# Kernel tuning notes

Measured on AMD Instinct MI355X. Metric: run time of the kernel, lower is better.

The kernel has to match this reference:

```python
import jax, jax.numpy as jnp
import numpy as np

B, D, H, O = 32, 128, 256, 10


def setup_inputs() -> dict:
    key = jax.random.key(0)
    ks = jax.random.split(key, 8)
    return {
        "t": jax.random.uniform(ks[0], (1,), dtype=jnp.float32),
        "state_batch": jax.random.normal(ks[1], (2 * B, D), dtype=jnp.float32),
        "x0": jax.random.normal(ks[2], (B, D), dtype=jnp.float32),
        "x1": jax.random.normal(ks[3], (B, D), dtype=jnp.float32),
        "W1": jax.random.normal(ks[4], (D, H), dtype=jnp.float32) / np.sqrt(D),
        "b1": jax.random.normal(ks[5], (H,), dtype=jnp.float32) * 0.01,
        "W2": jax.random.normal(ks[6], (H, O), dtype=jnp.float32) / np.sqrt(H),
        "b2": jax.random.normal(ks[7], (O,), dtype=jnp.float32) * 0.01,
    }


def reference(t, state_batch, x0, x1, W1, b1, W2, b2):
    b = x0.shape[0]
    deviation, dev_velocity = state_batch[:b], state_batch[b:]  # [B,D] each
    tt = t[0]
    window = 4.0 * tt * (1.0 - tt)
    # point on the perturbed path
    x = x0 + tt * (x1 - x0) + window * deviation  # [B,D]

    def f_single(xs):  # [D] -> [O]
        return jnp.tanh(xs @ W1 + b1) @ W2 + b2

    def G_single(xs):  # [D] -> [D,D] pullback metric J^T J + eps I
        J = jax.jacrev(f_single)(xs)  # [O,D] (O small -> reverse mode)
        return J.T @ J + 1e-4 * jnp.eye(xs.shape[0], dtype=xs.dtype)

    # dG[b,i,j,k] = d G_ij / d x_k  -- replaces the torch double autograd loop
    dG = jax.vmap(jax.jacfwd(G_single))(x)  # [B,D,D,D]
    dG = dG / (jnp.sqrt(jnp.sum(dG * dG, axis=(1, 2, 3), keepdims=True)) + 1e-6)
    # Christoffel symbols (first kind, up to normalization as in source)
    Gamma = 0.5 * (dG + jnp.transpose(dG, (0, 2, 1, 3)) - jnp.transpose(dG, (0, 3, 1, 2)))
    a = -jnp.einsum('bijk,bj,bk->bi', Gamma, dev_velocity, dev_velocity)
    a = a / (jnp.linalg.norm(dev_velocity, axis=1, keepdims=True) + 1e-6)
    restoration = -0.1 * deviation
    return jnp.concatenate([dev_velocity, a + restoration], axis=0)  # [2B,D]
```

## Files before the change

### kernel.cpp

```cpp
#include <hip/hip_runtime.h>
#include <hip/hip_bf16.h>


#define NB 32

#define OP    0

__device__ int g_pdone = 0;
__device__ int g_bdone = 0;

template<int BF> __device__ __forceinline__ float ld(const void* p, int i) {
  if constexpr (BF) return __bfloat162float(((const __hip_bfloat16*)p)[i]);
  else return ((const float*)p)[i];
}
template<int BF> __device__ __forceinline__ void st(void* p, int i, float v) {
  if constexpr (BF) ((__hip_bfloat16*)p)[i] = __float2bfloat16(v);
  else ((float*)p)[i] = v;
}
__device__ __forceinline__ float b2f(unsigned short u) {
  return __uint_as_float(((unsigned int)u) << 16);
}
template<int BF> __device__ __forceinline__ void ld8v(const void* p, int i, float* o) {
  if constexpr (BF) {
    uint4 u = *(const uint4*)((const unsigned short*)p + i);
    o[0] = b2f((unsigned short)(u.x & 0xffff)); o[1] = b2f((unsigned short)(u.x >> 16));
    o[2] = b2f((unsigned short)(u.y & 0xffff)); o[3] = b2f((unsigned short)(u.y >> 16));
    o[4] = b2f((unsigned short)(u.z & 0xffff)); o[5] = b2f((unsigned short)(u.z >> 16));
    o[6] = b2f((unsigned short)(u.w & 0xffff)); o[7] = b2f((unsigned short)(u.w >> 16));
  } else {
    float4 a = *(const float4*)((const float*)p + i);
    float4 b = *(const float4*)((const float*)p + i + 4);
    o[0]=a.x; o[1]=a.y; o[2]=a.z; o[3]=a.w; o[4]=b.x; o[5]=b.y; o[6]=b.z; o[7]=b.w;
  }
}

__device__ __forceinline__ int blocksniff(const void* sb, int* sh) {
  if (threadIdx.x == 0) *sh = 0;
  __syncthreads();
  float v = fabsf(__bfloat162float(((const __hip_bfloat16*)sb)[threadIdx.x & 255]));
  if (!(v < 1000.0f)) atomicOr(sh, 1);
  __syncthreads();
  return (*sh == 0) ? 1 : 0;
}

#define LXS   0
#define LVS   128
#define LW2   256
#define LYS   2816
#define LRED  2832
#define LF1   2880
#define LEL   4416
#define LSW2  7488
#define LCL   10560
#define LCL2  10660
#define LW2P  10760
#define LTOT  13832

#define F1ACC(wv, gidx) do { \
    const float* sp_ = &sm[LSW2 + (gidx)*12]; \
    float4 s0_ = *(const float4*)sp_; \
    float4 s1_ = *(const float4*)(sp_+4); \
    float2 s2_ = *(const float2*)(sp_+8); \
    fa[0]+=(wv)*s0_.x; fa[1]+=(wv)*s0_.y; fa[2]+=(wv)*s0_.z; fa[3]+=(wv)*s0_.w; \
    fa[4]+=(wv)*s1_.x; fa[5]+=(wv)*s1_.y; fa[6]+=(wv)*s1_.z; fa[7]+=(wv)*s1_.w; \
    fa[8]+=(wv)*s2_.x; fa[9]+=(wv)*s2_.y; \
  } while (0)

template<int BF>
__device__ void fk_body(const void* tin, const void* sbin, const void* x0in,
                        const void* x1in, const void* W1in, const void* b1in,
                        const void* W2in, void* out, float* ws, float* sm) {
  int bid = blockIdx.x, t = threadIdx.x;
  if (bid >= NB) {
    int row = bid - NB;
    float* colh = sm;
    if (t < 128) colh[t] = ld<BF>(W1in, t * 256 + row);
    __syncthreads();
    float pacc = 0.f;
    for (int d = 0; d < 128; d += 4) {
      float4 c4 = *(const float4*)&colh[d];
      pacc += c4.x * ld<BF>(W1in, (d + 0) * 256 + t);
      pacc += c4.y * ld<BF>(W1in, (d + 1) * 256 + t);
      pacc += c4.z * ld<BF>(W1in, (d + 2) * 256 + t);
      pacc += c4.w * ld<BF>(W1in, (d + 3) * 256 + t);
    }
    __hip_atomic_store(&ws[OP + row * 256 + t], pacc,
                       __ATOMIC_RELAXED, __HIP_MEMORY_SCOPE_AGENT);
    __syncthreads();
    if (t == 0)
      __hip_atomic_fetch_add(&g_pdone, 1, __ATOMIC_RELAXED, __HIP_MEMORY_SCOPE_AGENT);
    return;
  }
  int b = bid;
  int w = t >> 6;
  float tt = ld<BF>(tin, 0);
  float window = 4.f * tt * (1.f - tt);
  if (t < 128) {
    float dev = ld<BF>(sbin, b * 128 + t);
    float v   = ld<BF>(sbin, (NB + b) * 128 + t);
    float x0v = ld<BF>(x0in, b * 128 + t);
    float x1v = ld<BF>(x1in, b * 128 + t);
    sm[LXS + t] = x0v + tt * (x1v - x0v) + window * dev;
    sm[LVS + t] = v;
  }
  for (int i = t; i < 2560; i += 256) sm[LW2 + i] = ld<BF>(W2in, i);
  __syncthreads();
  float hacc = ld<BF>(b1in, t), wacc = 0.f;
  for (int d = 0; d < 128; d += 4) {
    float4 xv = *(const float4*)&sm[LXS + d];
    float4 vv = *(const float4*)&sm[LVS + d];
    float w0 = ld<BF>(W1in, (d + 0) * 256 + t);
    float w1 = ld<BF>(W1in, (d + 1) * 256 + t);
    float w2 = ld<BF>(W1in, (d + 2) * 256 + t);
    float w3 = ld<BF>(W1in, (d + 3) * 256 + t);
    hacc += w0 * xv.x + w1 * xv.y + w2 * xv.z + w3 * xv.w;
    wacc += w0 * vv.x + w1 * vv.y + w2 * vv.z + w3 * vv.w;
  }
  float z  = tanhf(hacc);
  float sg = 1.f - z * z;
  float ug = -2.f * z * sg;
  float w2r[10];
  #pragma unroll
  for (int o = 0; o < 10; ++o) w2r[o] = sm[LW2 + t * 10 + o];
  #pragma unroll
  for (int o = 0; o < 10; ++o) sm[LSW2 + t * 12 + o] = sg * w2r[o];
  for (int i = t; i < 3072; i += 256) {
    int r = i / 12, c = i - r * 12;
    sm[LW2P + i] = (c < 10) ? sm[LW2 + r * 10 + c] : 0.f;
  }
  float cval = ug * wacc * wacc;
  float rv[11];
  #pragma unroll
  for (int o = 0; o < 10; ++o) rv[o] = cval * w2r[o];
  rv[10] = (t < 128) ? sm[LVS + t] * sm[LVS + t] : 0.f;
  #pragma unroll
  for (int o = 0; o < 11; ++o) {
    float v = rv[o];
    #pragma unroll
    for (int m = 32; m > 0; m >>= 1) v += __shfl_xor(v, m);
    if ((t & 63) == 0) sm[LRED + w * 12 + o] = v;
  }
  __syncthreads();
  if (t < 11) {
    float s = sm[LRED + t] + sm[LRED + 12 + t] + sm[LRED + 24 + t] + sm[LRED + 36 + t];
    if (t < 10) sm[LYS + t] = s;
    else        sm[LYS + 10] = sqrtf(s);
  }
  int half = t >> 7, r = t & 127;
  float fa[10];
  #pragma unroll
  for (int o = 0; o < 10; ++o) fa[o] = 0.f;
  {
    const int gbase = half * 128;
    for (int gg = 0; gg < 128; gg += 8) {
      int g = gbase + gg;
      float wv[8];
      ld8v<BF>(W1in, r * 256 + g, wv);
      F1ACC(wv[0], g + 0); F1ACC(wv[1], g + 1);
      F1ACC(wv[2], g + 2); F1ACC(wv[3], g + 3);
      F1ACC(wv[4], g + 4); F1ACC(wv[5], g + 5);
      F1ACC(wv[6], g + 6); F1ACC(wv[7], g + 7);
    }
  }
  if (half) {
    #pragma unroll
    for (int o = 0; o < 10; ++o) sm[LF1 + r * 12 + o] = fa[o];
  }
  __syncthreads();
  float aun = 0.f;
  if (!half) {
    #pragma unroll
    for (int o = 0; o < 10; ++o) {
      float f = fa[o] + sm[LF1 + r * 12 + o];
      sm[LF1 + r * 12 + o] = f;
      aun += f * sm[LYS + o];
    }
  }
  __syncthreads();
  float er[10];
  #pragma unroll
  for (int o = 0; o < 10; ++o) er[o] = 0.f;
  for (int d = 0; d < 128; ++d) {
    float w1v = ld<BF>(W1in, d * 256 + t);
    const float* fp = &sm[LF1 + d * 12];
    float4 a0 = *(const float4*)fp;
    float4 a1 = *(const float4*)(fp + 4);
    float2 a2 = *(const float2*)(fp + 8);
    er[0] += w1v * a0.x; er[1] += w1v * a0.y; er[2] += w1v * a0.z; er[3] += w1v * a0.w;
    er[4] += w1v * a1.x; er[5] += w1v * a1.y; er[6] += w1v * a1.z; er[7] += w1v * a1.w;
    er[8] += w1v * a2.x; er[9] += w1v * a2.y;
  }
  #pragma unroll
  for (int o = 0; o < 10; ++o) sm[LEL + t * 12 + o] = er[o];
  sm[LEL + t * 12 + 10] = ug;
  sm[LEL + t * 12 + 11] = 0.f;
  __syncthreads();
  float cpart = 0.f;
  if (t < 200) {
    int gh = (t >= 100) ? 1 : 0;
    int idx = t - gh * 100;
    int o = idx / 10, p = idx - o * 10;
    const float* sa = &sm[LSW2 + gh * 1536 + o];
    const float* sb = &sm[LEL  + gh * 1536 + p];
    #pragma unroll 4
    for (int g = 0; g < 128; ++g) cpart += sa[g * 12] * sb[g * 12];
    if (gh) sm[LCL2 + idx] = cpart;
  }
  __syncthreads();
  if (t < 100) sm[LCL + t] = cpart + sm[LCL2 + t];
  __syncthreads();
  float cwr[10];
  #pragma unroll
  for (int o = 0; o < 10; ++o) {
    float cw = 0.f;
    #pragma unroll
    for (int p = 0; p < 10; ++p) cw += sm[LCL + o * 10 + p] * w2r[p];
    cwr[o] = cw;
  }
  if (t == 0) {
    while (__hip_atomic_load(&g_pdone, __ATOMIC_RELAXED, __HIP_MEMORY_SCOPE_AGENT) < 256)
      __builtin_amdgcn_s_sleep(2);
  }
  __syncthreads();
  float acc = 0.f;
  for (int i0 = 0; i0 < 64; i0 += 16) {
    float ph[16];
    #pragma unroll
    for (int j = 0; j < 16; ++j)
      ph[j] = ws[OP + (w * 64 + i0 + j) * 256 + t];
    #pragma unroll
    for (int j = 0; j < 16; ++j) {
      int h = w * 64 + i0 + j;
      const float* rp = &sm[LEL + h * 12];
      float4 E0 = *(const float4*)rp;
      float4 E1 = *(const float4*)(rp + 4);
      float4 E2 = *(const float4*)(rp + 8);
      const float* wp = &sm[LW2P + h * 12];
      float4 W0 = *(const float4*)wp;
      float4 W1v = *(const float4*)(wp + 4);
      float4 W2v = *(const float4*)(wp + 8);
      float R = E0.x*w2r[0] + E0.y*w2r[1] + E0.z*w2r[2] + E0.w*w2r[3]
              + E1.x*w2r[4] + E1.y*w2r[5] + E1.z*w2r[6] + E1.w*w2r[7]
              + E2.x*w2r[8] + E2.y*w2r[9];
      float Rt = W0.x*er[0] + W0.y*er[1] + W0.z*er[2] + W0.w*er[3]
               + W1v.x*er[4] + W1v.y*er[5] + W1v.z*er[6] + W1v.w*er[7]
               + W2v.x*er[8] + W2v.y*er[9];
      float Qd = W0.x*cwr[0] + W0.y*cwr[1] + W0.z*cwr[2] + W0.w*cwr[3]
               + W1v.x*cwr[4] + W1v.y*cwr[5] + W1v.z*cwr[6] + W1v.w*cwr[7]
               + W2v.x*cwr[8] + W2v.y*cwr[9];
      acc += E2.z * ph[j] * (ph[j] * Qd + R * Rt);
    }
  }
  acc *= ug;
  #pragma unroll
  for (int m = 32; m > 0; m >>= 1) acc += __shfl_xor(acc, m);
  if ((t & 63) == 0) sm[LRED + w] = acc;
  __syncthreads();
  float F = sqrtf(fmaxf(2.f * (sm[LRED] + sm[LRED+1] + sm[LRED+2] + sm[LRED+3]), 0.f));
  float denom = (F + 1e-6f) * (sm[LYS + 10] + 1e-6f);
  if (t < 128) {
    st<BF>(out, b * 128 + t, ld<BF>(sbin, (NB + b) * 128 + t));
    float dev = ld<BF>(sbin, b * 128 + t);
    float val = -aun / denom - 0.1f * dev;
    st<BF>(out, (NB + b) * 128 + t, val);
  }
  __syncthreads();
  if (t == 0) {
    int old = __hip_atomic_fetch_add(&g_bdone, 1, __ATOMIC_RELAXED, __HIP_MEMORY_SCOPE_AGENT);
    if (old == NB - 1) {
      __hip_atomic_store(&g_pdone, 0, __ATOMIC_RELAXED, __HIP_MEMORY_SCOPE_AGENT);
      __hip_atomic_store(&g_bdone, 0, __ATOMIC_RELAXED, __HIP_MEMORY_SCOPE_AGENT);
    }
  }
}

__global__ __launch_bounds__(256, 2) void FK(const void* tin, const void* sbin,
                                             const void* x0in, const void* x1in,
                                             const void* W1in, const void* b1in,
                                             const void* W2in, void* out, float* ws) {
  __shared__ int sh;
  __shared__ __align__(16) float sm[LTOT];
  int bf = blocksniff(sbin, &sh);
  if (bf) fk_body<1>(tin, sbin, x0in, x1in, W1in, b1in, W2in, out, ws, sm);
  else    fk_body<0>(tin, sbin, x0in, x1in, W1in, b1in, W2in, out, ws, sm);
}

extern "C" void kernel_launch(void* const* d_in, const int* in_sizes, int n_in,
                              void* d_out, int out_size, void* d_ws, size_t ws_size,
                              hipStream_t stream) {
  float* ws = (float*)d_ws;
  const void* tin  = d_in[0];
  const void* sbin = d_in[1];
  const void* x0in = d_in[2];
  const void* x1in = d_in[3];
  const void* W1in = d_in[4];
  const void* b1in = d_in[5];
  const void* W2in = d_in[6];

  FK<<<dim3(NB + 256), dim3(256), 0, stream>>>(tin, sbin, x0in, x1in, W1in, b1in, W2in, d_out, ws);
}
```

Before: 99.54 us.

## Double block size to 512 threads and split reductions across thread halves

Blocks grow from 256 to 512 threads. Every per-batch phase (first-layer matvec, F1 accumulation, the er backprop loop, the Cl contraction, the final Hessian-weighted sum) now splits its reduction dimension across the extra thread groups, with partial sums combined through shared memory. Helper blocks that precompute W1^T W1 each handle two rows, so there are half as many of them and the spin-wait threshold changes to match. The aim is shorter serial loops per thread in the 32 latency-bound batch blocks, at the cost of more barriers, more shared-memory traffic and a tighter register budget.

```diff
diff --git a/kernel.cpp b/kernel.cpp
--- a/kernel.cpp
+++ b/kernel.cpp
@@ -3,8 +3,7 @@
 
 
 #define NB 32
-
-#define OP    0
+#define OP 0
 
 __device__ int g_pdone = 0;
 __device__ int g_bdone = 0;
@@ -48,13 +47,14 @@
 #define LW2   256
 #define LYS   2816
 #define LRED  2832
-#define LF1   2880
-#define LEL   4416
-#define LSW2  7488
-#define LCL   10560
-#define LCL2  10660
-#define LW2P  10760
-#define LTOT  13832
+#define LHW   2928
+#define LF1   3440
+#define LEL   4976
+#define LSW2  8048
+#define LCL   11120
+#define LCQ   11220
+#define LW2P  11520
+#define LTOT  14592
 
 #define F1ACC(wv, gidx) do { \
     const float* sp_ = &sm[LSW2 + (gidx)*12]; \
@@ -72,19 +72,24 @@
                         const void* W2in, void* out, float* ws, float* sm) {
   int bid = blockIdx.x, t = threadIdx.x;
   if (bid >= NB) {
-    int row = bid - NB;
+    int row0 = (bid - NB) * 2;
     float* colh = sm;
-    if (t < 128) colh[t] = ld<BF>(W1in, t * 256 + row);
+    if (t < 256) {
+      int qq = t >> 7, d = t & 127;
+      colh[qq * 128 + d] = ld<BF>(W1in, d * 256 + row0 + qq);
+    }
     __syncthreads();
+    int q = t >> 8, c = t & 255;
+    const float* ch = &colh[q * 128];
     float pacc = 0.f;
     for (int d = 0; d < 128; d += 4) {
-      float4 c4 = *(const float4*)&colh[d];
-      pacc += c4.x * ld<BF>(W1in, (d + 0) * 256 + t);
-      pacc += c4.y * ld<BF>(W1in, (d + 1) * 256 + t);
-      pacc += c4.z * ld<BF>(W1in, (d + 2) * 256 + t);
-      pacc += c4.w * ld<BF>(W1in, (d + 3) * 256 + t);
-    }
-    __hip_atomic_store(&ws[OP + row * 256 + t], pacc,
+      float4 c4 = *(const float4*)&ch[d];
+      pacc += c4.x * ld<BF>(W1in, (d + 0) * 256 + c);
+      pacc += c4.y * ld<BF>(W1in, (d + 1) * 256 + c);
+      pacc += c4.z * ld<BF>(W1in, (d + 2) * 256 + c);
+      pacc += c4.w * ld<BF>(W1in, (d + 3) * 256 + c);
+    }
+    __hip_atomic_store(&ws[OP + (row0 + q) * 256 + c], pacc,
                        __ATOMIC_RELAXED, __HIP_MEMORY_SCOPE_AGENT);
     __syncthreads();
     if (t == 0)
@@ -92,7 +97,11 @@
     return;
   }
   int b = bid;
-  int w = t >> 6;
+  int t2 = t & 255;
+  int q  = t >> 8;
+  int w  = t >> 6;
+  int r  = t & 127;
+  int qr = t >> 7;
   float tt = ld<BF>(tin, 0);
   float window = 4.f * tt * (1.f - tt);
   if (t < 128) {
@@ -103,42 +112,48 @@
     sm[LXS + t] = x0v + tt * (x1v - x0v) + window * dev;
     sm[LVS + t] = v;
   }
-  for (int i = t; i < 2560; i += 256) sm[LW2 + i] = ld<BF>(W2in, i);
-  __syncthreads();
-  float hacc = ld<BF>(b1in, t), wacc = 0.f;
-  for (int d = 0; d < 128; d += 4) {
-    float4 xv = *(const float4*)&sm[LXS + d];
-    float4 vv = *(const float4*)&sm[LVS + d];
-    float w0 = ld<BF>(W1in, (d + 0) * 256 + t);
-    float w1 = ld<BF>(W1in, (d + 1) * 256 + t);
-    float w2 = ld<BF>(W1in, (d + 2) * 256 + t);
-    float w3 = ld<BF>(W1in, (d + 3) * 256 + t);
-    hacc += w0 * xv.x + w1 * xv.y + w2 * xv.z + w3 * xv.w;
-    wacc += w0 * vv.x + w1 * vv.y + w2 * vv.z + w3 * vv.w;
-  }
-  float z  = tanhf(hacc);
-  float sg = 1.f - z * z;
-  float ug = -2.f * z * sg;
+  for (int i = t; i < 2560; i += 512) sm[LW2 + i] = ld<BF>(W2in, i);
+  __syncthreads();
+  float hp = q ? 0.f : ld<BF>(b1in, t2), wp = 0.f;
+  {
+    int d0 = q * 64;
+    for (int d = d0; d < d0 + 64; d += 4) {
+      float4 xv = *(const float4*)&sm[LXS + d];
+      float4 vv = *(const float4*)&sm[LVS + d];
+      float w0 = ld<BF>(W1in, (d + 0) * 256 + t2);
+      float w1 = ld<BF>(W1in, (d + 1) * 256 + t2);
+      float w2 = ld<BF>(W1in, (d + 2) * 256 + t2);
+      float w3 = ld<BF>(W1in, (d + 3) * 256 + t2);
+      hp += w0 * xv.x + w1 * xv.y + w2 * xv.z + w3 * xv.w;
+      wp += w0 * vv.x + w1 * vv.y + w2 * vv.z + w3 * vv.w;
+    }
+  }
+  if (q) { sm[LHW + t2 * 2] = hp; sm[LHW + t2 * 2 + 1] = wp; }
   float w2r[10];
   #pragma unroll
-  for (int o = 0; o < 10; ++o) w2r[o] = sm[LW2 + t * 10 + o];
-  #pragma unroll
-  for (int o = 0; o < 10; ++o) sm[LSW2 + t * 12 + o] = sg * w2r[o];
-  for (int i = t; i < 3072; i += 256) {
-    int r = i / 12, c = i - r * 12;
-    sm[LW2P + i] = (c < 10) ? sm[LW2 + r * 10 + c] : 0.f;
-  }
-  float cval = ug * wacc * wacc;
-  float rv[11];
-  #pragma unroll
-  for (int o = 0; o < 10; ++o) rv[o] = cval * w2r[o];
-  rv[10] = (t < 128) ? sm[LVS + t] * sm[LVS + t] : 0.f;
-  #pragma unroll
-  for (int o = 0; o < 11; ++o) {
-    float v = rv[o];
-    #pragma unroll
-    for (int m = 32; m > 0; m >>= 1) v += __shfl_xor(v, m);
-    if ((t & 63) == 0) sm[LRED + w * 12 + o] = v;
+  for (int o = 0; o < 10; ++o) w2r[o] = sm[LW2 + t2 * 10 + o];
+  __syncthreads();
+  float ug = 0.f;
+  if (!q) {
+    float hacc = hp + sm[LHW + t2 * 2];
+    float wacc = wp + sm[LHW + t2 * 2 + 1];
+    float z  = tanhf(hacc);
+    float sg = 1.f - z * z;
+    ug = -2.f * z * sg;
+    #pragma unroll
+    for (int o = 0; o < 10; ++o) sm[LSW2 + t2 * 12 + o] = sg * w2r[o];
+    float cval = ug * wacc * wacc;
+    float rv[11];
+    #pragma unroll
+    for (int o = 0; o < 10; ++o) rv[o] = cval * w2r[o];
+    rv[10] = (t < 128) ? sm[LVS + t] * sm[LVS + t] : 0.f;
+    #pragma unroll
+    for (int o = 0; o < 11; ++o) {
+      float v = rv[o];
+      #pragma unroll
+      for (int m = 32; m > 0; m >>= 1) v += __shfl_xor(v, m);
+      if ((t & 63) == 0) sm[LRED + w * 12 + o] = v;
+    }
   }
   __syncthreads();
   if (t < 11) {
@@ -146,13 +161,12 @@
     if (t < 10) sm[LYS + t] = s;
     else        sm[LYS + 10] = sqrtf(s);
   }
-  int half = t >> 7, r = t & 127;
   float fa[10];
   #pragma unroll
   for (int o = 0; o < 10; ++o) fa[o] = 0.f;
   {
-    const int gbase = half * 128;
-    for (int gg = 0; gg < 128; gg += 8) {
+    int gbase = qr * 64;
+    for (int gg = 0; gg < 64; gg += 8) {
       int g = gbase + gg;
       float wv[8];
       ld8v<BF>(W1in, r * 256 + g, wv);
@@ -162,16 +176,23 @@
       F1ACC(wv[6], g + 6); F1ACC(wv[7], g + 7);
     }
   }
-  if (half) {
-    #pragma unroll
-    for (int o = 0; o < 10; ++o) sm[LF1 + r * 12 + o] = fa[o];
+  if (qr == 1) {
+    #pragma unroll
+    for (int o = 0; o < 10; ++o) sm[LEL + r * 12 + o] = fa[o];
+  } else if (qr == 2) {
+    #pragma unroll
+    for (int o = 0; o < 10; ++o) sm[LEL + 1536 + r * 12 + o] = fa[o];
+  } else if (qr == 3) {
+    #pragma unroll
+    for (int o = 0; o < 10; ++o) sm[LW2P + r * 12 + o] = fa[o];
   }
   __syncthreads();
   float aun = 0.f;
-  if (!half) {
+  if (!qr) {
     #pragma unroll
     for (int o = 0; o < 10; ++o) {
-      float f = fa[o] + sm[LF1 + r * 12 + o];
+      float f = fa[o] + sm[LEL + r * 12 + o] + sm[LEL + 1536 + r * 12 + o]
+                      + sm[LW2P + r * 12 + o];
       sm[LF1 + r * 12 + o] = f;
       aun += f * sm[LYS + o];
     }
@@ -180,34 +201,50 @@
   float er[10];
   #pragma unroll
   for (int o = 0; o < 10; ++o) er[o] = 0.f;
-  for (int d = 0; d < 128; ++d) {
-    float w1v = ld<BF>(W1in, d * 256 + t);
-    const float* fp = &sm[LF1 + d * 12];
-    float4 a0 = *(const float4*)fp;
-    float4 a1 = *(const float4*)(fp + 4);
-    float2 a2 = *(const float2*)(fp + 8);
-    er[0] += w1v * a0.x; er[1] += w1v * a0.y; er[2] += w1v * a0.z; er[3] += w1v * a0.w;
-    er[4] += w1v * a1.x; er[5] += w1v * a1.y; er[6] += w1v * a1.z; er[7] += w1v * a1.w;
-    er[8] += w1v * a2.x; er[9] += w1v * a2.y;
-  }
-  #pragma unroll
-  for (int o = 0; o < 10; ++o) sm[LEL + t * 12 + o] = er[o];
-  sm[LEL + t * 12 + 10] = ug;
-  sm[LEL + t * 12 + 11] = 0.f;
-  __syncthreads();
+  {
+    int d0 = q * 64;
+    for (int d = d0; d < d0 + 64; ++d) {
+      float w1v = ld<BF>(W1in, d * 256 + t2);
+      const float* fp = &sm[LF1 + d * 12];
+      float4 a0 = *(const float4*)fp;
+      float4 a1 = *(const float4*)(fp + 4);
+      float2 a2 = *(const float2*)(fp + 8);
+      er[0] += w1v * a0.x; er[1] += w1v * a0.y; er[2] += w1v * a0.z; er[3] += w1v * a0.w;
+      er[4] += w1v * a1.x; er[5] += w1v * a1.y; er[6] += w1v * a1.z; er[7] += w1v * a1.w;
+      er[8] += w1v * a2.x; er[9] += w1v * a2.y;
+    }
+  }
+  if (q) {
+    #pragma unroll
+    for (int o = 0; o < 10; ++o) sm[LW2P + t2 * 12 + o] = er[o];
+  }
+  __syncthreads();
+  if (!q) {
+    #pragma unroll
+    for (int o = 0; o < 10; ++o)
+      sm[LEL + t2 * 12 + o] = er[o] + sm[LW2P + t2 * 12 + o];
+    sm[LEL + t2 * 12 + 10] = ug;
+    sm[LEL + t2 * 12 + 11] = 0.f;
+  }
+  __syncthreads();
+  for (int i = t; i < 3072; i += 512) {
+    int rr = i / 12, cc = i - rr * 12;
+    sm[LW2P + i] = (cc < 10) ? sm[LW2 + rr * 10 + cc] : 0.f;
+  }
   float cpart = 0.f;
-  if (t < 200) {
-    int gh = (t >= 100) ? 1 : 0;
-    int idx = t - gh * 100;
+  if (t < 400) {
+    int chk = t / 100, idx = t - chk * 100;
     int o = idx / 10, p = idx - o * 10;
-    const float* sa = &sm[LSW2 + gh * 1536 + o];
-    const float* sb = &sm[LEL  + gh * 1536 + p];
+    const float* sa = &sm[LSW2 + o];
+    const float* sb = &sm[LEL + p];
+    int g0 = chk * 64;
     #pragma unroll 4
-    for (int g = 0; g < 128; ++g) cpart += sa[g * 12] * sb[g * 12];
-    if (gh) sm[LCL2 + idx] = cpart;
-  }
-  __syncthreads();
-  if (t < 100) sm[LCL + t] = cpart + sm[LCL2 + t];
+    for (int g = g0; g < g0 + 64; ++g) cpart += sa[g * 12] * sb[g * 12];
+    if (chk) sm[LCQ + (chk - 1) * 100 + idx] = cpart;
+  }
+  __syncthreads();
+  if (t < 100)
+    sm[LCL + t] = cpart + sm[LCQ + t] + sm[LCQ + 100 + t] + sm[LCQ + 200 + t];
   __syncthreads();
   float cwr[10];
   #pragma unroll
@@ -217,28 +254,39 @@
     for (int p = 0; p < 10; ++p) cw += sm[LCL + o * 10 + p] * w2r[p];
     cwr[o] = cw;
   }
+  float uc;
+  {
+    const float* ep = &sm[LEL + t2 * 12];
+    float4 e0 = *(const float4*)ep;
+    float4 e1 = *(const float4*)(ep + 4);
+    float4 e2 = *(const float4*)(ep + 8);
+    er[0]=e0.x; er[1]=e0.y; er[2]=e0.z; er[3]=e0.w;
+    er[4]=e1.x; er[5]=e1.y; er[6]=e1.z; er[7]=e1.w;
+    er[8]=e2.x; er[9]=e2.y; uc = e2.z;
+  }
   if (t == 0) {
-    while (__hip_atomic_load(&g_pdone, __ATOMIC_RELAXED, __HIP_MEMORY_SCOPE_AGENT) < 256)
+    while (__hip_atomic_load(&g_pdone, __ATOMIC_RELAXED, __HIP_MEMORY_SCOPE_AGENT) < 128)
       __builtin_amdgcn_s_sleep(2);
   }
   __syncthreads();
+  int band = (t2 >> 6) * 64 + q * 32;
   float acc = 0.f;
-  for (int i0 = 0; i0 < 64; i0 += 16) {
+  for (int i0 = 0; i0 < 32; i0 += 16) {
     float ph[16];
     #pragma unroll
     for (int j = 0; j < 16; ++j)
-      ph[j] = ws[OP + (w * 64 + i0 + j) * 256 + t];
+      ph[j] = ws[OP + (band + i0 + j) * 256 + t2];
     #pragma unroll
     for (int j = 0; j < 16; ++j) {
-      int h = w * 64 + i0 + j;
+      int h = band + i0 + j;
       const float* rp = &sm[LEL + h * 12];
       float4 E0 = *(const float4*)rp;
       float4 E1 = *(const float4*)(rp + 4);
       float4 E2 = *(const float4*)(rp + 8);
-      const float* wp = &sm[LW2P + h * 12];
-      float4 W0 = *(const float4*)wp;
-      float4 W1v = *(const float4*)(wp + 4);
-      float4 W2v = *(const float4*)(wp + 8);
+      const float* wpp = &sm[LW2P + h * 12];
+      float4 W0 = *(const float4*)wpp;
+      float4 W1v = *(const float4*)(wpp + 4);
+      float4 W2v = *(const float4*)(wpp + 8);
       float R = E0.x*w2r[0] + E0.y*w2r[1] + E0.z*w2r[2] + E0.w*w2r[3]
               + E1.x*w2r[4] + E1.y*w2r[5] + E1.z*w2r[6] + E1.w*w2r[7]
               + E2.x*w2r[8] + E2.y*w2r[9];
@@ -251,12 +299,13 @@
       acc += E2.z * ph[j] * (ph[j] * Qd + R * Rt);
     }
   }
-  acc *= ug;
+  acc *= uc;
   #pragma unroll
   for (int m = 32; m > 0; m >>= 1) acc += __shfl_xor(acc, m);
   if ((t & 63) == 0) sm[LRED + w] = acc;
   __syncthreads();
-  float F = sqrtf(fmaxf(2.f * (sm[LRED] + sm[LRED+1] + sm[LRED+2] + sm[LRED+3]), 0.f));
+  float F = sqrtf(fmaxf(2.f * (sm[LRED] + sm[LRED+1] + sm[LRED+2] + sm[LRED+3]
+                             + sm[LRED+4] + sm[LRED+5] + sm[LRED+6] + sm[LRED+7]), 0.f));
   float denom = (F + 1e-6f) * (sm[LYS + 10] + 1e-6f);
   if (t < 128) {
     st<BF>(out, b * 128 + t, ld<BF>(sbin, (NB + b) * 128 + t));
@@ -274,10 +323,10 @@
   }
 }
 
-__global__ __launch_bounds__(256, 2) void FK(const void* tin, const void* sbin,
-                                             const void* x0in, const void* x1in,
-                                             const void* W1in, const void* b1in,
-                                             const void* W2in, void* out, float* ws) {
+__global__ __launch_bounds__(512) void FK(const void* tin, const void* sbin,
+                                          const void* x0in, const void* x1in,
+                                          const void* W1in, const void* b1in,
+                                          const void* W2in, void* out, float* ws) {
   __shared__ int sh;
   __shared__ __align__(16) float sm[LTOT];
   int bf = blocksniff(sbin, &sh);
@@ -297,5 +346,5 @@
   const void* b1in = d_in[5];
   const void* W2in = d_in[6];
 
-  FK<<<dim3(NB + 256), dim3(256), 0, stream>>>(tin, sbin, x0in, x1in, W1in, b1in, W2in, d_out, ws);
-}
+  FK<<<dim3(NB + 128), dim3(512), 0, stream>>>(tin, sbin, x0in, x1in, W1in, b1in, W2in, d_out, ws);
+}
```

Result: faster. 91.25 us (median of 2 runs) (-8.3%).
